# Kernel tuning notes

Hardware: AMD Instinct MI355X
Metric: run time of the kernel (lower is better)

Reference implementation:

```python
import jax, jax.numpy as jnp
import numpy as np

B, T, D = 4, 4096, 1024
EPS = 1e-5  # FusedRMSNormSwishGate default eps


def setup_inputs() -> dict:
    key = jax.random.key(0)
    ks = jax.random.split(key, 6)
    s = 1.0 / np.sqrt(D)
    return {
        "x": jax.random.normal(ks[0], (B, T, D), jnp.float32),
        "Wi": jax.random.normal(ks[1], (D, D), jnp.float32) * s,
        "Wf": jax.random.normal(ks[2], (D, D), jnp.float32) * s,
        "Wg": jax.random.normal(ks[3], (D, D), jnp.float32) * s,
        "Wo": jax.random.normal(ks[4], (D, D), jnp.float32) * s,
        "norm_w": jnp.ones((D,), jnp.float32),
    }


def _hgrn_scan(f, i):
    # h_t = f_t * h_{t-1} + i_t  (elementwise gated linear recurrence)
    # associative combine: (f1,i1) o (f2,i2) = (f1*f2, i1*f2 + i2)
    def combine(a, b):
        fa, ia = a
        fb, ib = b
        return fa * fb, ia * fb + ib

    _, h = jax.lax.associative_scan(combine, (f, i), axis=1)
    return h


def reference(x, Wi, Wf, Wg, Wo, norm_w):
    # projections
    i = x @ Wi.T                                  # [B,T,D]
    f = jax.nn.sigmoid(x @ Wf.T)                  # forget gate in (0,1)
    # swiglu(i, 1-f): silu on the value, gated by the input gate (1-f)
    inp = jax.nn.silu(i) * (1.0 - f)
    # hierarchically-gated linear recurrence (chunk/parallel scan form)
    h = _hgrn_scan(f, inp)                        # [B,T,D]
    # RMSNorm(h) * swish(g) output gate
    g = x @ Wg.T
    rms = h * jax.lax.rsqrt(jnp.mean(h * h, axis=-1, keepdims=True) + EPS)
    o = (rms * norm_w) * (g * jax.nn.sigmoid(g))
    return o @ Wo.T
```

## Files before the change

kernel.cpp:

```cpp
#include <hip/hip_runtime.h>
#include <hip/hip_bf16.h>

typedef unsigned short u16;
using bf16x8 = __bf16 __attribute__((ext_vector_type(8)));
using f32x4  = float  __attribute__((ext_vector_type(4)));

#define BB 4
#define TT 4096
#define DD 1024
#define MROWS (BB*TT)
#define CT 64
#define NC (TT/CT)

__device__ __forceinline__ float sigm(float x) { return 1.0f / (1.0f + __expf(-x)); }
__device__ __forceinline__ u16 f2bf(float f) {
    __hip_bfloat16 h = __float2bfloat16(f);
    return *reinterpret_cast<u16*>(&h);
}
__device__ __forceinline__ float bf2f(u16 u) { return __uint_as_float(((unsigned)u) << 16); }

__device__ __forceinline__ void async_cp16(const u16* g, u16* l) {
    __builtin_amdgcn_global_load_lds(
        (const __attribute__((address_space(1))) unsigned int*)g,
        (__attribute__((address_space(3))) unsigned int*)l, 16, 0, 0);
}

__global__ __launch_bounds__(256) void conv_x_kernel(const float* __restrict__ s,
                                                     u16* __restrict__ d) {
    size_t i = (size_t)blockIdx.x * 256 + threadIdx.x;
    float4 v = *(const float4*)(s + i * 4);
    ushort4 u;
    u.x = f2bf(v.x); u.y = f2bf(v.y); u.z = f2bf(v.z); u.w = f2bf(v.w);
    *(ushort4*)(d + i * 4) = u;
}

__global__ __launch_bounds__(256) void conv_w4_kernel(const float* __restrict__ w0,
                                                      const float* __restrict__ w1,
                                                      const float* __restrict__ w2,
                                                      const float* __restrict__ w3,
                                                      u16* __restrict__ dst) {
    int i = blockIdx.x * 256 + threadIdx.x;
    int sel = i >> 18;
    int off = i & 262143;
    const float* s = (sel == 0) ? w0 : (sel == 1) ? w1 : (sel == 2) ? w2 : w3;
    float4 v = *(const float4*)(s + (size_t)off * 4);
    ushort4 u;
    u.x = f2bf(v.x); u.y = f2bf(v.y); u.z = f2bf(v.z); u.w = f2bf(v.w);
    *(ushort4*)(dst + ((size_t)sel << 20) + (size_t)off * 4) = u;
}

#define BM 128
#define BN 128
#define BK 64

template <typename OutT>
__global__ __launch_bounds__(256, 2)
void gemm_bf16_bt(const u16* __restrict__ Ag, const u16* __restrict__ Bg, int K,
                  OutT* __restrict__ P0, OutT* __restrict__ P1, OutT* __restrict__ P2) {
    __shared__ u16 As[BM * BK];
    __shared__ u16 Bs[BN * BK];

    const int tid  = threadIdx.x;
    const int lane = tid & 63;
    const int wid  = tid >> 6;
    const int wm   = wid >> 1;
    const int wn   = wid & 1;
    const int lr   = lane & 15;
    const int lq   = lane >> 4;

    const long bM  = (long)blockIdx.y * BM;
    const long bN0 = (long)blockIdx.x * BN;

    const f32x4 zero = {0.f, 0.f, 0.f, 0.f};
    f32x4 acc[4][4];
#pragma unroll
    for (int i = 0; i < 4; i++)
#pragma unroll
        for (int j = 0; j < 4; j++) acc[i][j] = zero;

    for (int kt = 0; kt < K; kt += BK) {
        __syncthreads();
#pragma unroll
        for (int j = 0; j < 4; j++) {
            const int G  = j * 256 + tid;
            const int m  = G >> 3;
            const int p  = G & 7;
            const int gk = p ^ (m & 7);
            async_cp16(Ag + (bM + m) * K + kt + gk * 8, &As[G * 8]);
            async_cp16(Bg + (bN0 + m) * K + kt + gk * 8, &Bs[G * 8]);
        }
        __syncthreads();
#pragma unroll
        for (int kk = 0; kk < BK / 32; kk++) {
            bf16x8 av[4], bv[4];
#pragma unroll
            for (int f = 0; f < 4; f++) {
                const int am = wm * 64 + f * 16 + lr;
                const int ag = (kk * 4 + lq) ^ (am & 7);
                av[f] = *(const bf16x8*)(&As[am * 64 + ag * 8]);
                const int bn = wn * 64 + f * 16 + lr;
                const int bg = (kk * 4 + lq) ^ (bn & 7);
                bv[f] = *(const bf16x8*)(&Bs[bn * 64 + bg * 8]);
            }
#pragma unroll
            for (int i = 0; i < 4; i++)
#pragma unroll
                for (int j = 0; j < 4; j++)
                    acc[i][j] = __builtin_amdgcn_mfma_f32_16x16x32_bf16(av[i], bv[j],
                                                                        acc[i][j], 0, 0, 0);
        }
    }

    const int pl = (int)(bN0 >> 10);
    OutT* P = (pl == 0) ? P0 : ((pl == 1) ? P1 : P2);
    const int cn = (int)(bN0 & 1023);
#pragma unroll
    for (int i = 0; i < 4; i++) {
        const long m0 = bM + wm * 64 + i * 16 + lq * 4;
#pragma unroll
        for (int j = 0; j < 4; j++) {
            const int n = cn + wn * 64 + j * 16 + lr;
#pragma unroll
            for (int r = 0; r < 4; r++) {
                if constexpr (sizeof(OutT) == 2)
                    P[(m0 + r) * 1024 + n] = f2bf(acc[i][j][r]);
                else
                    P[(m0 + r) * 1024 + n] = acc[i][j][r];
            }
        }
    }
}

__global__ __launch_bounds__(256) void scan_pass1(const u16* __restrict__ ip,
                                                  const u16* __restrict__ fp,
                                                  float* __restrict__ Fc,
                                                  float* __restrict__ Ic) {
    const int tid = blockIdx.x * 256 + threadIdx.x;
    const int d = tid & 1023;
    const int c = (tid >> 10) & (NC - 1);
    const int b = tid >> 16;
    size_t base = ((size_t)(b * TT + c * CT) << 10) + d;
    float F = 1.f, I = 0.f;
#pragma unroll 8
    for (int t = 0; t < CT; t++) {
        float fv = bf2f(fp[base]);
        float iv = bf2f(ip[base]);
        base += DD;
        float f = sigm(fv);
        float v = iv * sigm(iv) * (1.f - f);
        I = fmaf(f, I, v);
        F *= f;
    }
    Fc[tid] = F;
    Ic[tid] = I;
}

__global__ __launch_bounds__(256) void scan_pass2(const float* __restrict__ Fc,
                                                  const float* __restrict__ Ic,
                                                  float* __restrict__ Hin) {
    const int tid = blockIdx.x * 256 + threadIdx.x;
    const int d = tid & 1023;
    const int b = tid >> 10;
    float H = 0.f;
    for (int c = 0; c < NC; c++) {
        const int idx = ((b * NC + c) << 10) + d;
        Hin[idx] = H;
        H = fmaf(Fc[idx], H, Ic[idx]);
    }
}

__global__ __launch_bounds__(256) void scan_pass3(const u16* __restrict__ ip,
                                                  const u16* __restrict__ fp,
                                                  const float* __restrict__ Hin,
                                                  u16* __restrict__ hout) {
    const int tid = blockIdx.x * 256 + threadIdx.x;
    const int d = tid & 1023;
    const int c = (tid >> 10) & (NC - 1);
    const int b = tid >> 16;
    size_t base = ((size_t)(b * TT + c * CT) << 10) + d;
    float h = Hin[tid];
#pragma unroll 8
    for (int t = 0; t < CT; t++) {
        float fv = bf2f(fp[base]);
        float iv = bf2f(ip[base]);
        float f = sigm(fv);
        float v = iv * sigm(iv) * (1.f - f);
        h = fmaf(f, h, v);
        hout[base] = f2bf(h);
        base += DD;
    }
}

__global__ __launch_bounds__(256) void rmsnorm_gate(const u16* hin,
                                                    const u16* __restrict__ g,
                                                    const float* __restrict__ w,
                                                    u16* oout) {
    const int row = blockIdx.x;
    const int t = threadIdx.x;
    const size_t base = ((size_t)row << 10) + t * 4;
    ushort4 hu = *(const ushort4*)(hin + base);
    float h0 = bf2f(hu.x), h1 = bf2f(hu.y), h2 = bf2f(hu.z), h3 = bf2f(hu.w);
    float ss = h0 * h0 + h1 * h1 + h2 * h2 + h3 * h3;
#pragma unroll
    for (int o = 32; o > 0; o >>= 1) ss += __shfl_down(ss, o);
    __shared__ float red[4];
    if ((t & 63) == 0) red[t >> 6] = ss;
    __syncthreads();
    const float tot = red[0] + red[1] + red[2] + red[3];
    const float rms = rsqrtf(tot * (1.f / 1024.f) + 1e-5f);
    ushort4 gu = *(const ushort4*)(g + base);
    float g0 = bf2f(gu.x), g1 = bf2f(gu.y), g2 = bf2f(gu.z), g3 = bf2f(gu.w);
    float4 wv = *(const float4*)(w + (size_t)t * 4);
    ushort4 ou;
    ou.x = f2bf(h0 * rms * wv.x * g0 * sigm(g0));
    ou.y = f2bf(h1 * rms * wv.y * g1 * sigm(g1));
    ou.z = f2bf(h2 * rms * wv.z * g2 * sigm(g2));
    ou.w = f2bf(h3 * rms * wv.w * g3 * sigm(g3));
    *(ushort4*)(oout + base) = ou;
}

extern "C" void kernel_launch(void* const* d_in, const int* in_sizes, int n_in,
                              void* d_out, int out_size, void* d_ws, size_t ws_size,
                              hipStream_t stream) {
    const float* x  = (const float*)d_in[0];
    const float* Wi = (const float*)d_in[1];
    const float* Wf = (const float*)d_in[2];
    const float* Wg = (const float*)d_in[3];
    const float* Wo = (const float*)d_in[4];
    const float* nw = (const float*)d_in[5];
    float* out = (float*)d_out;

    const size_t MB = 1ull << 20;
    char* ws = (char*)d_ws;
    u16*   xo  = (u16*)(ws);
    u16*   Wb  = (u16*)(ws + 32 * MB);
    u16*   Pi  = (u16*)(ws + 40 * MB);
    u16*   Pf  = (u16*)(ws + 72 * MB);
    float* Fc  = (float*)(ws + 104 * MB);
    float* Ic  = Fc + BB * NC * DD;
    float* Hin = Ic + BB * NC * DD;
    u16*   g   = (u16*)d_out;

    conv_x_kernel<<<16384, 256, 0, stream>>>(x, xo);
    conv_w4_kernel<<<4096, 256, 0, stream>>>(Wi, Wf, Wg, Wo, Wb);
    gemm_bf16_bt<u16><<<dim3(24, 128), 256, 0, stream>>>(xo, Wb, 1024, Pi, Pf, g);
    scan_pass1<<<1024, 256, 0, stream>>>(Pi, Pf, Fc, Ic);
    scan_pass2<<<16, 256, 0, stream>>>(Fc, Ic, Hin);
    scan_pass3<<<1024, 256, 0, stream>>>(Pi, Pf, Hin, xo);
    rmsnorm_gate<<<16384, 256, 0, stream>>>(xo, g, nw, xo);
    gemm_bf16_bt<float><<<dim3(8, 128), 256, 0, stream>>>(xo, Wb + 3ull * 1024 * 1024, 1024,
                                                          out, out, out);
}
```

Measured before the change: 364.7 us.

## Fuse scan pass3 with RMSNorm gate, merge conversions, vectorize scan passes

Merges the x and weight bf16 conversions into one launch. Fuses the third scan pass with the RMSNorm and swish gate into a single 1024-thread-per-block kernel that does a per-timestep block reduction, so the intermediate h tensor is never written and read back. Vectorizes scan passes 1 and 2 to four channels per thread, halves the chunk length to 32, and raises the GEMM launch-bounds occupancy hint. The fused kernel adds a __syncthreads per timestep and has far fewer resident blocks, so it may lose memory-level parallelism. The higher occupancy hint may force register spills in the GEMM.

```diff
diff --git a/kernel.cpp b/kernel.cpp
--- a/kernel.cpp
+++ b/kernel.cpp
@@ -9,7 +9,7 @@
 #define TT 4096
 #define DD 1024
 #define MROWS (BB*TT)
-#define CT 64
+#define CT 32
 #define NC (TT/CT)
 
 __device__ __forceinline__ float sigm(float x) { return 1.0f / (1.0f + __expf(-x)); }
@@ -25,28 +25,31 @@
         (__attribute__((address_space(3))) unsigned int*)l, 16, 0, 0);
 }
 
-__global__ __launch_bounds__(256) void conv_x_kernel(const float* __restrict__ s,
-                                                     u16* __restrict__ d) {
-    size_t i = (size_t)blockIdx.x * 256 + threadIdx.x;
-    float4 v = *(const float4*)(s + i * 4);
+__global__ __launch_bounds__(256) void prep_kernel(const float* __restrict__ x,
+                                                   const float* __restrict__ w0,
+                                                   const float* __restrict__ w1,
+                                                   const float* __restrict__ w2,
+                                                   const float* __restrict__ w3,
+                                                   u16* __restrict__ xo,
+                                                   u16* __restrict__ Wb) {
+    const int i = blockIdx.x * 256 + threadIdx.x;
+    const float* s;
+    u16* d;
+    if (i < 4194304) {
+        s = x + (size_t)i * 4;
+        d = xo + (size_t)i * 4;
+    } else {
+        const int j = i - 4194304;
+        const int sel = j >> 18;
+        const int off = j & 262143;
+        const float* w = (sel == 0) ? w0 : (sel == 1) ? w1 : (sel == 2) ? w2 : w3;
+        s = w + (size_t)off * 4;
+        d = Wb + ((size_t)sel << 20) + (size_t)off * 4;
+    }
+    float4 v = *(const float4*)s;
     ushort4 u;
     u.x = f2bf(v.x); u.y = f2bf(v.y); u.z = f2bf(v.z); u.w = f2bf(v.w);
-    *(ushort4*)(d + i * 4) = u;
-}
-
-__global__ __launch_bounds__(256) void conv_w4_kernel(const float* __restrict__ w0,
-                                                      const float* __restrict__ w1,
-                                                      const float* __restrict__ w2,
-                                                      const float* __restrict__ w3,
-                                                      u16* __restrict__ dst) {
-    int i = blockIdx.x * 256 + threadIdx.x;
-    int sel = i >> 18;
-    int off = i & 262143;
-    const float* s = (sel == 0) ? w0 : (sel == 1) ? w1 : (sel == 2) ? w2 : w3;
-    float4 v = *(const float4*)(s + (size_t)off * 4);
-    ushort4 u;
-    u.x = f2bf(v.x); u.y = f2bf(v.y); u.z = f2bf(v.z); u.w = f2bf(v.w);
-    *(ushort4*)(dst + ((size_t)sel << 20) + (size_t)off * 4) = u;
+    *(ushort4*)d = u;
 }
 
 #define BM 128
@@ -54,7 +57,7 @@
 #define BK 64
 
 template <typename OutT>
-__global__ __launch_bounds__(256, 2)
+__global__ __launch_bounds__(256, 4)
 void gemm_bf16_bt(const u16* __restrict__ Ag, const u16* __restrict__ Bg, int K,
                   OutT* __restrict__ P0, OutT* __restrict__ P1, OutT* __restrict__ P2) {
     __shared__ u16 As[BM * BK];
@@ -135,88 +138,87 @@
                                                   const u16* __restrict__ fp,
                                                   float* __restrict__ Fc,
                                                   float* __restrict__ Ic) {
-    const int tid = blockIdx.x * 256 + threadIdx.x;
-    const int d = tid & 1023;
-    const int c = (tid >> 10) & (NC - 1);
-    const int b = tid >> 16;
-    size_t base = ((size_t)(b * TT + c * CT) << 10) + d;
-    float F = 1.f, I = 0.f;
-#pragma unroll 8
+    const int q  = blockIdx.x * 256 + threadIdx.x;
+    const int d4 = q & 255;
+    const int c  = (q >> 8) & (NC - 1);
+    const int b  = q >> 15;
+    size_t base = ((size_t)(b * TT + c * CT) << 10) + d4 * 4;
+    float4 F = {1.f, 1.f, 1.f, 1.f};
+    float4 I = {0.f, 0.f, 0.f, 0.f};
+#pragma unroll 4
     for (int t = 0; t < CT; t++) {
-        float fv = bf2f(fp[base]);
-        float iv = bf2f(ip[base]);
+        ushort4 fu = *(const ushort4*)(fp + base);
+        ushort4 iu = *(const ushort4*)(ip + base);
         base += DD;
-        float f = sigm(fv);
-        float v = iv * sigm(iv) * (1.f - f);
-        I = fmaf(f, I, v);
-        F *= f;
-    }
-    Fc[tid] = F;
-    Ic[tid] = I;
+        float f0 = sigm(bf2f(fu.x)), f1 = sigm(bf2f(fu.y)),
+              f2 = sigm(bf2f(fu.z)), f3 = sigm(bf2f(fu.w));
+        float i0 = bf2f(iu.x), i1 = bf2f(iu.y), i2 = bf2f(iu.z), i3 = bf2f(iu.w);
+        I.x = fmaf(f0, I.x, i0 * sigm(i0) * (1.f - f0));
+        I.y = fmaf(f1, I.y, i1 * sigm(i1) * (1.f - f1));
+        I.z = fmaf(f2, I.z, i2 * sigm(i2) * (1.f - f2));
+        I.w = fmaf(f3, I.w, i3 * sigm(i3) * (1.f - f3));
+        F.x *= f0; F.y *= f1; F.z *= f2; F.w *= f3;
+    }
+    const size_t o = ((size_t)((b * NC + c) << 10)) + d4 * 4;
+    *(float4*)(Fc + o) = F;
+    *(float4*)(Ic + o) = I;
 }
 
 __global__ __launch_bounds__(256) void scan_pass2(const float* __restrict__ Fc,
                                                   const float* __restrict__ Ic,
                                                   float* __restrict__ Hin) {
-    const int tid = blockIdx.x * 256 + threadIdx.x;
-    const int d = tid & 1023;
-    const int b = tid >> 10;
-    float H = 0.f;
+    const int q  = blockIdx.x * 256 + threadIdx.x;
+    const int d4 = q & 255;
+    const int b  = q >> 8;
+    float4 H = {0.f, 0.f, 0.f, 0.f};
     for (int c = 0; c < NC; c++) {
-        const int idx = ((b * NC + c) << 10) + d;
-        Hin[idx] = H;
-        H = fmaf(Fc[idx], H, Ic[idx]);
-    }
-}
-
-__global__ __launch_bounds__(256) void scan_pass3(const u16* __restrict__ ip,
-                                                  const u16* __restrict__ fp,
-                                                  const float* __restrict__ Hin,
-                                                  u16* __restrict__ hout) {
-    const int tid = blockIdx.x * 256 + threadIdx.x;
-    const int d = tid & 1023;
-    const int c = (tid >> 10) & (NC - 1);
-    const int b = tid >> 16;
-    size_t base = ((size_t)(b * TT + c * CT) << 10) + d;
-    float h = Hin[tid];
-#pragma unroll 8
-    for (int t = 0; t < CT; t++) {
-        float fv = bf2f(fp[base]);
-        float iv = bf2f(ip[base]);
-        float f = sigm(fv);
-        float v = iv * sigm(iv) * (1.f - f);
-        h = fmaf(f, h, v);
-        hout[base] = f2bf(h);
+        const size_t idx = ((size_t)((b * NC + c) << 10)) + d4 * 4;
+        float4 F = *(const float4*)(Fc + idx);
+        float4 I = *(const float4*)(Ic + idx);
+        *(float4*)(Hin + idx) = H;
+        H.x = fmaf(F.x, H.x, I.x);
+        H.y = fmaf(F.y, H.y, I.y);
+        H.z = fmaf(F.z, H.z, I.z);
+        H.w = fmaf(F.w, H.w, I.w);
+    }
+}
+
+__global__ __launch_bounds__(1024) void scan_finalize(const u16* __restrict__ ip,
+                                                      const u16* __restrict__ fp,
+                                                      const float* __restrict__ Hin,
+                                                      const u16* __restrict__ g,
+                                                      const float* __restrict__ w,
+                                                      u16* __restrict__ oout) {
+    const int t  = threadIdx.x;
+    const int c  = blockIdx.x & (NC - 1);
+    const int b  = blockIdx.x >> 7;
+    const int lane = t & 63;
+    const int wid  = t >> 6;
+    __shared__ float red[2][16];
+
+    size_t base = ((size_t)(b * TT + c * CT) << 10) + t;
+    float h = Hin[((size_t)((b * NC + c) << 10)) + t];
+    const float wn = w[t];
+
+    for (int tt = 0; tt < CT; tt++) {
+        const float fv = bf2f(fp[base]);
+        const float iv = bf2f(ip[base]);
+        const float gv = bf2f(g[base]);
+        const float f = sigm(fv);
+        h = fmaf(f, h, iv * sigm(iv) * (1.f - f));
+        float ss = h * h;
+#pragma unroll
+        for (int o = 32; o > 0; o >>= 1) ss += __shfl_down(ss, o);
+        const int pb = tt & 1;
+        if (lane == 0) red[pb][wid] = ss;
+        __syncthreads();
+        float tot = 0.f;
+#pragma unroll
+        for (int k = 0; k < 16; k++) tot += red[pb][k];
+        const float rms = rsqrtf(tot * (1.f / 1024.f) + 1e-5f);
+        oout[base] = f2bf(h * rms * wn * gv * sigm(gv));
         base += DD;
     }
-}
-
-__global__ __launch_bounds__(256) void rmsnorm_gate(const u16* hin,
-                                                    const u16* __restrict__ g,
-                                                    const float* __restrict__ w,
-                                                    u16* oout) {
-    const int row = blockIdx.x;
-    const int t = threadIdx.x;
-    const size_t base = ((size_t)row << 10) + t * 4;
-    ushort4 hu = *(const ushort4*)(hin + base);
-    float h0 = bf2f(hu.x), h1 = bf2f(hu.y), h2 = bf2f(hu.z), h3 = bf2f(hu.w);
-    float ss = h0 * h0 + h1 * h1 + h2 * h2 + h3 * h3;
-#pragma unroll
-    for (int o = 32; o > 0; o >>= 1) ss += __shfl_down(ss, o);
-    __shared__ float red[4];
-    if ((t & 63) == 0) red[t >> 6] = ss;
-    __syncthreads();
-    const float tot = red[0] + red[1] + red[2] + red[3];
-    const float rms = rsqrtf(tot * (1.f / 1024.f) + 1e-5f);
-    ushort4 gu = *(const ushort4*)(g + base);
-    float g0 = bf2f(gu.x), g1 = bf2f(gu.y), g2 = bf2f(gu.z), g3 = bf2f(gu.w);
-    float4 wv = *(const float4*)(w + (size_t)t * 4);
-    ushort4 ou;
-    ou.x = f2bf(h0 * rms * wv.x * g0 * sigm(g0));
-    ou.y = f2bf(h1 * rms * wv.y * g1 * sigm(g1));
-    ou.z = f2bf(h2 * rms * wv.z * g2 * sigm(g2));
-    ou.w = f2bf(h3 * rms * wv.w * g3 * sigm(g3));
-    *(ushort4*)(oout + base) = ou;
 }
 
 extern "C" void kernel_launch(void* const* d_in, const int* in_sizes, int n_in,
@@ -237,17 +239,15 @@
     u16*   Pi  = (u16*)(ws + 40 * MB);
     u16*   Pf  = (u16*)(ws + 72 * MB);
     float* Fc  = (float*)(ws + 104 * MB);
-    float* Ic  = Fc + BB * NC * DD;
-    float* Hin = Ic + BB * NC * DD;
+    float* Ic  = (float*)(ws + 106 * MB);
+    float* Hin = (float*)(ws + 108 * MB);
     u16*   g   = (u16*)d_out;
 
-    conv_x_kernel<<<16384, 256, 0, stream>>>(x, xo);
-    conv_w4_kernel<<<4096, 256, 0, stream>>>(Wi, Wf, Wg, Wo, Wb);
+    prep_kernel<<<20480, 256, 0, stream>>>(x, Wi, Wf, Wg, Wo, xo, Wb);
     gemm_bf16_bt<u16><<<dim3(24, 128), 256, 0, stream>>>(xo, Wb, 1024, Pi, Pf, g);
-    scan_pass1<<<1024, 256, 0, stream>>>(Pi, Pf, Fc, Ic);
-    scan_pass2<<<16, 256, 0, stream>>>(Fc, Ic, Hin);
-    scan_pass3<<<1024, 256, 0, stream>>>(Pi, Pf, Hin, xo);
-    rmsnorm_gate<<<16384, 256, 0, stream>>>(xo, g, nw, xo);
+    scan_pass1<<<512, 256, 0, stream>>>(Pi, Pf, Fc, Ic);
+    scan_pass2<<<4, 256, 0, stream>>>(Fc, Ic, Hin);
+    scan_finalize<<<512, 1024, 0, stream>>>(Pi, Pf, Hin, g, nw, xo);
     gemm_bf16_bt<float><<<dim3(8, 128), 256, 0, stream>>>(xo, Wb + 3ull * 1024 * 1024, 1024,
                                                           out, out, out);
 }
```

Result: no change. 365.3 us (+0.2%).
